# Kernel optimization log

Measured on AMD Instinct MI355X. Metric: run time of the kernel, lower is better.

## Reference

```python
import jax, jax.numpy as jnp
import numpy as np

B, N, R = 4, 16, 64        # batch, permuted axis size, inner spatial size
M, S = N // 2, R * 2       # block count, block size


def _glorot(key, shape):
    fan_in, fan_out = shape[-2], shape[-1]
    lim = np.sqrt(6.0 / (fan_in + fan_out)).astype(np.float32)
    return jax.random.uniform(key, shape, jnp.float32, -lim, lim)


def setup_inputs() -> dict:
    key = jax.random.key(0)
    ks = jax.random.split(key, 10)
    inp = {
        "x": jax.random.normal(ks[0], (B, N, R, N, R, 2), jnp.float32),
        "perm_idx": jax.random.permutation(ks[1], N).astype(jnp.int32),
    }
    for i, name in enumerate(["hr1", "hi1", "hr2", "hi2", "hr3", "hi3", "hr4", "hi4"]):
        inp[name] = _glorot(ks[2 + i], (M, S, S))
    return inp


def _bilin(v, p_right, p_left):
    # v: (B, m, s, m, s). First contract the last s-axis against p_right's
    # block matmuls (block index = axis 3), then the axis-2 s-axis against
    # p_left's block matmuls (block index = axis 1).
    t = jnp.einsum('bmiaj,ajk->bmiak', v, p_right)
    return jnp.einsum('xbjci,bjk->xbkci', t, p_left)


def reference(x, perm_idx, hr1, hi1, hr2, hi2, hr3, hi3, hr4, hi4):
    m = x.shape[1] // 2
    s = x.shape[2] * 2
    n, r = m * 2, s // 2
    x = x.take(perm_idx, axis=1).take(perm_idx, axis=3)
    x = x.reshape((-1, m, s, m, s, 2))
    x_re, x_im = x[..., 0], x[..., 1]

    y_re = (_bilin(x_re, hr1, hr1) + _bilin(x_re, hi1, hi1)
            + _bilin(x_im, hi2, hr2) + _bilin(x_im, hr2, hi2))
    y_im = (_bilin(x_im, hr3, hr3) + _bilin(x_im, hi3, hi3)
            + _bilin(x_re, hi4, hr4) + _bilin(x_re, hr4, hi4))

    y = jnp.stack([y_re, y_im], axis=-1)
    return y.reshape((-1, n, r, n, r, 2))
```

## Files before the change

kernel.cpp:

```cpp
#include <hip/hip_runtime.h>
#include <hip/hip_bf16.h>
#include <stdint.h>

typedef __attribute__((ext_vector_type(8))) short bf16x8;
typedef __attribute__((ext_vector_type(4))) float f32x4;
typedef __attribute__((ext_vector_type(16))) float f32x16;

#define MFMA32(a, b, c) __builtin_amdgcn_mfma_f32_32x32x16_bf16((a), (b), (c), 0, 0, 0)

__device__ __forceinline__ unsigned short f2bf_rn(float f) {
    union { __bf16 b; unsigned short u; } v;
    v.b = (__bf16)f;
    return v.u;
}

__device__ __forceinline__ unsigned int pk2(float lo, float hi) {
    union { unsigned short s[2]; unsigned int u; } r;
    r.s[0] = f2bf_rn(lo); r.s[1] = f2bf_rn(hi);
    return r.u;
}

__device__ __forceinline__ void gload_lds16(const void* g, void* l) {
    __builtin_amdgcn_global_load_lds(
        (const __attribute__((address_space(1))) void*)g,
        (__attribute__((address_space(3))) void*)l, 16, 0, 0);
}

__global__ __launch_bounds__(256) void prep_h(
    const float* __restrict__ h0, const float* __restrict__ h1,
    const float* __restrict__ h2, const float* __restrict__ h3,
    const float* __restrict__ h4, const float* __restrict__ h5,
    const float* __restrict__ h6, const float* __restrict__ h7,
    unsigned short* __restrict__ ht)
{
    const float* hmap[8] = {h0, h1, h2, h3, h4, h5, h6, h7};
    const int wg = blockIdx.x;
    const int jblk = wg >> 2, qt = wg & 3;
    const float* src = hmap[jblk >> 3] + (jblk & 7) * 16384;
    unsigned short* dst = ht + jblk * 16384;
    __shared__ unsigned short tile[32 * 129];
    const int t = threadIdx.x;
    #pragma unroll
    for (int i = 0; i < 16; ++i) {
        int idx = t + 256 * i;
        int r = idx >> 5, kk = idx & 31;
        tile[kk * 129 + r] = f2bf_rn(src[r * 128 + qt * 32 + kk]);
    }
    __syncthreads();
    #pragma unroll
    for (int i = 0; i < 16; ++i) {
        int idx = t + 256 * i;
        int k = idx >> 7, r = idx & 127;
        dst[(qt * 32 + k) * 128 + r] = tile[k * 129 + r];
    }
}

__global__ __launch_bounds__(512, 2) void bilin_main(
    const float* __restrict__ x, const int* __restrict__ perm,
    const unsigned short* __restrict__ ht, float* __restrict__ out)
{
    const int wg = blockIdx.x;
    const int q = wg & 7, p = (wg >> 3) & 7, b = wg >> 6;
    const int tid = threadIdx.x;
    const int lane = tid & 63, wid = tid >> 6;
    const int wn = wid & 3, h = wid >> 2;
    const int l31 = lane & 31, hl = lane >> 5;

    __shared__ __align__(16) unsigned short smem[81920];
    unsigned short* xlds = smem;

    constexpr int cseq[8]  = {0, 1, 6, 7, 2, 3, 4, 5};
    constexpr int rperm[8] = {0, 1, 3, 2, 4, 5, 7, 6};

    const int n1a = perm[2 * p], n1b = perm[2 * p + 1];
    const int n2a = perm[2 * q], n2b = perm[2 * q + 1];

    const int wubase = tid & ~63;
    auto stage_h = [&](unsigned short* dst, int blk) {
        const unsigned short* src = ht + blk * 16384;
        #pragma unroll
        for (int r = 0; r < 4; ++r) {
            const int idx = r * 512 + tid;
            const int row = idx >> 4, cin = idx & 15;
            gload_lds16(src + row * 128 + ((cin ^ (row & 15)) << 3),
                        dst + ((r * 512 + wubase) << 3));
        }
    };

    auto stage_x = [&](int g) {
        float4 xv[4][4];
        int woffs[4];
        #pragma unroll
        for (int i = 0; i < 4; ++i) {
            const int idx = i * 512 + tid;
            const int row = idx >> 4, cin = idx & 15;
            const int n1 = (i >> 1) ? n1b : n1a;
            const int n2 = (cin >> 3) ? n2b : n2a;
            const int r1 = row & 63, r2 = (cin & 7) * 8;
            const float* sp = x + ((size_t)((b * 16 + n1) * 64 + r1) * 1024
                                   + n2 * 64 + r2) * 2;
            #pragma unroll
            for (int j = 0; j < 4; ++j)
                xv[i][j] = *(const float4*)(sp + j * 4);
            woffs[i] = row * 128 + ((cin ^ (row & 15)) << 3);
        }
        #pragma unroll
        for (int i = 0; i < 4; ++i) {
            bf16x8 t;
            #pragma unroll
            for (int j = 0; j < 4; ++j) {
                if (g == 0) {
                    t[2 * j]     = (short)f2bf_rn(xv[i][j].x);
                    t[2 * j + 1] = (short)f2bf_rn(xv[i][j].z);
                } else {
                    t[2 * j]     = (short)f2bf_rn(xv[i][j].y);
                    t[2 * j + 1] = (short)f2bf_rn(xv[i][j].w);
                }
            }
            *(bf16x8*)(xlds + woffs[i]) = t;
        }
    };

    auto ldr = [&](const unsigned short* base, int row, int ch) -> bf16x8 {
        return *(const bf16x8*)(base + row * 128 + ((ch ^ (row & 15)) << 3));
    };

    stage_h(smem + 16384, rperm[0] * 8 + q);
    stage_h(smem + 49152, 0 * 8 + p);
    stage_x(0);
    __syncthreads();

    f32x16 yre[4], yim[4];
    #pragma unroll
    for (int i = 0; i < 4; ++i) {
        #pragma unroll
        for (int e = 0; e < 16; ++e) { yre[i][e] = 0.f; yim[i][e] = 0.f; }
    }

    #pragma unroll
    for (int cc = 0; cc < 8; ++cc) {
        const unsigned short* wb = smem + 16384 + (cc & 1) * 16384;
        const unsigned short* lb = smem + 49152 + (cc & 1) * 16384;

        if (cc < 7) {
            stage_h(smem + 16384 + ((cc + 1) & 1) * 16384,
                    rperm[cseq[cc + 1]] * 8 + q);
            stage_h(smem + 49152 + ((cc + 1) & 1) * 16384,
                    cseq[cc + 1] * 8 + p);
        }

        f32x16 u[2];
        #pragma unroll
        for (int e = 0; e < 16; ++e) { u[0][e] = 0.f; u[1][e] = 0.f; }
        #pragma unroll
        for (int ks = 0; ks < 8; ++ks) {
            bf16x8 wfr = ldr(wb, wn * 32 + l31, 2 * ks + hl);
            #pragma unroll
            for (int m2 = 0; m2 < 2; ++m2) {
                bf16x8 xfr = ldr(xlds, h * 64 + m2 * 32 + l31, 2 * ks + hl);
                u[m2] = MFMA32(xfr, wfr, u[m2]);
            }
        }

        #pragma unroll
        for (int t = 0; t < 4; ++t) {
            const int f = t >> 1, qa = (t & 1) * 2, qb = qa + 1;
            unsigned int lo0 = pk2(u[f][4 * qa + 0], u[f][4 * qa + 1]);
            unsigned int lo1 = pk2(u[f][4 * qa + 2], u[f][4 * qa + 3]);
            unsigned int hi0 = pk2(u[f][4 * qb + 0], u[f][4 * qb + 1]);
            unsigned int hi1 = pk2(u[f][4 * qb + 2], u[f][4 * qb + 3]);
            unsigned int send0 = hl ? lo0 : hi0;
            unsigned int send1 = hl ? lo1 : hi1;
            unsigned int sx0 = (unsigned int)__shfl_xor((int)send0, 32);
            unsigned int sx1 = (unsigned int)__shfl_xor((int)send1, 32);
            union { unsigned int d[4]; bf16x8 v; } ufu;
            ufu.d[0] = hl ? sx0 : lo0;
            ufu.d[1] = hl ? sx1 : lo1;
            ufu.d[2] = hl ? hi0 : sx0;
            ufu.d[3] = hl ? hi1 : sx1;
            #pragma unroll
            for (int mt = 0; mt < 4; ++mt) {
                bf16x8 lfr = ldr(lb, mt * 32 + l31, 8 * h + 2 * t + hl);
                if ((cc & 3) < 2) yre[mt] = MFMA32(lfr, ufu.v, yre[mt]);
                else              yim[mt] = MFMA32(lfr, ufu.v, yim[mt]);
            }
        }

        if (cc == 3) {
            __syncthreads();
            stage_x(1);
        }

        __syncthreads();
    }

    float* red = (float*)smem + wn * 8192;
    if (h == 1) {
        #pragma unroll
        for (int mt = 0; mt < 4; ++mt)
            #pragma unroll
            for (int q4 = 0; q4 < 4; ++q4) {
                f32x4 vr, vi;
                #pragma unroll
                for (int jj = 0; jj < 4; ++jj) {
                    vr[jj] = yre[mt][4 * q4 + jj];
                    vi[jj] = yim[mt][4 * q4 + jj];
                }
                *(f32x4*)(red + ((0 * 4 + mt) * 4 + q4) * 256 + lane * 4) = vr;
                *(f32x4*)(red + ((1 * 4 + mt) * 4 + q4) * 256 + lane * 4) = vi;
            }
    }
    __syncthreads();
    if (h == 0) {
        float2* o2 = (float2*)out;
        #pragma unroll
        for (int mt = 0; mt < 4; ++mt)
            #pragma unroll
            for (int q4 = 0; q4 < 4; ++q4) {
                f32x4 pr = *(const f32x4*)(red + ((0 * 4 + mt) * 4 + q4) * 256 + lane * 4);
                f32x4 pi = *(const f32x4*)(red + ((1 * 4 + mt) * 4 + q4) * 256 + lane * 4);
                #pragma unroll
                for (int jj = 0; jj < 4; ++jj) {
                    const int j = 4 * q4 + jj;
                    const int row = mt * 32 + (j & 3) + 8 * (j >> 2) + 4 * hl;
                    float2 v;
                    v.x = yre[mt][j] + pr[jj];
                    v.y = yim[mt][j] + pi[jj];
                    o2[(size_t)(b * 1024 + p * 128 + row) * 1024
                       + q * 128 + wn * 32 + l31] = v;
                }
            }
    }
}

extern "C" void kernel_launch(void* const* d_in, const int* in_sizes, int n_in,
                              void* d_out, int out_size, void* d_ws, size_t ws_size,
                              hipStream_t stream) {
    const float* x  = (const float*)d_in[0];
    const int* perm = (const int*)d_in[1];
    unsigned short* htp = (unsigned short*)d_ws;

    hipLaunchKernelGGL(prep_h, dim3(256), dim3(256), 0, stream,
        (const float*)d_in[2], (const float*)d_in[3], (const float*)d_in[4],
        (const float*)d_in[5], (const float*)d_in[6], (const float*)d_in[7],
        (const float*)d_in[8], (const float*)d_in[9], htp);
    hipLaunchKernelGGL(bilin_main, dim3(256), dim3(512), 0, stream,
        x, perm, htp, (float*)d_out);
}
```

Before: 40.18 us.

## Use 4-wave workgroups without split-K reduction, register-cached x fragments

Halves the workgroup to 4 waves so each wave computes the full K range for its column strip, which removes the LDS cross-wave reduction at the end. Both real and imaginary x planes are staged once into LDS. The x fragments are held in registers across the loop, reloaded once at the switch to the imaginary plane. The left-matrix buffer is single-buffered and restaged after an extra barrier each iteration. This trades fewer waves per CU and serialized left-matrix loads for less LDS traffic and no reduction pass, and the large register footprint risks spills.

```diff
diff --git a/kernel.cpp b/kernel.cpp
--- a/kernel.cpp
+++ b/kernel.cpp
@@ -55,80 +55,83 @@
     }
 }
 
-__global__ __launch_bounds__(512, 2) void bilin_main(
+__global__ __launch_bounds__(256, 1) void bilin_main(
     const float* __restrict__ x, const int* __restrict__ perm,
     const unsigned short* __restrict__ ht, float* __restrict__ out)
 {
     const int wg = blockIdx.x;
     const int q = wg & 7, p = (wg >> 3) & 7, b = wg >> 6;
     const int tid = threadIdx.x;
-    const int lane = tid & 63, wid = tid >> 6;
-    const int wn = wid & 3, h = wid >> 2;
+    const int lane = tid & 63, wn = tid >> 6;
     const int l31 = lane & 31, hl = lane >> 5;
 
     __shared__ __align__(16) unsigned short smem[81920];
-    unsigned short* xlds = smem;
+    unsigned short* xre_lds = smem;
+    unsigned short* xim_lds = smem + 16384;
+    unsigned short* llds = smem + 65536;
 
     constexpr int cseq[8]  = {0, 1, 6, 7, 2, 3, 4, 5};
     constexpr int rperm[8] = {0, 1, 3, 2, 4, 5, 7, 6};
-
-    const int n1a = perm[2 * p], n1b = perm[2 * p + 1];
-    const int n2a = perm[2 * q], n2b = perm[2 * q + 1];
 
     const int wubase = tid & ~63;
     auto stage_h = [&](unsigned short* dst, int blk) {
         const unsigned short* src = ht + blk * 16384;
         #pragma unroll
-        for (int r = 0; r < 4; ++r) {
-            const int idx = r * 512 + tid;
+        for (int r = 0; r < 8; ++r) {
+            const int idx = r * 256 + tid;
             const int row = idx >> 4, cin = idx & 15;
             gload_lds16(src + row * 128 + ((cin ^ (row & 15)) << 3),
-                        dst + ((r * 512 + wubase) << 3));
-        }
-    };
-
-    auto stage_x = [&](int g) {
-        float4 xv[4][4];
-        int woffs[4];
-        #pragma unroll
-        for (int i = 0; i < 4; ++i) {
-            const int idx = i * 512 + tid;
+                        dst + ((r * 256 + wubase) << 3));
+        }
+    };
+
+    auto ldr = [&](const unsigned short* base, int row, int ch) -> bf16x8 {
+        return *(const bf16x8*)(base + row * 128 + ((ch ^ (row & 15)) << 3));
+    };
+
+    auto stage_x_both = [&]() {
+        #pragma unroll
+        for (int i = 0; i < 8; ++i) {
+            const int idx = i * 256 + tid;
             const int row = idx >> 4, cin = idx & 15;
-            const int n1 = (i >> 1) ? n1b : n1a;
-            const int n2 = (cin >> 3) ? n2b : n2a;
+            const int n1 = perm[2 * p + (row >> 6)];
+            const int n2 = perm[2 * q + (cin >> 3)];
             const int r1 = row & 63, r2 = (cin & 7) * 8;
             const float* sp = x + ((size_t)((b * 16 + n1) * 64 + r1) * 1024
                                    + n2 * 64 + r2) * 2;
-            #pragma unroll
-            for (int j = 0; j < 4; ++j)
-                xv[i][j] = *(const float4*)(sp + j * 4);
-            woffs[i] = row * 128 + ((cin ^ (row & 15)) << 3);
-        }
-        #pragma unroll
-        for (int i = 0; i < 4; ++i) {
-            bf16x8 t;
-            #pragma unroll
-            for (int j = 0; j < 4; ++j) {
-                if (g == 0) {
-                    t[2 * j]     = (short)f2bf_rn(xv[i][j].x);
-                    t[2 * j + 1] = (short)f2bf_rn(xv[i][j].z);
-                } else {
-                    t[2 * j]     = (short)f2bf_rn(xv[i][j].y);
-                    t[2 * j + 1] = (short)f2bf_rn(xv[i][j].w);
-                }
-            }
-            *(bf16x8*)(xlds + woffs[i]) = t;
-        }
-    };
-
-    auto ldr = [&](const unsigned short* base, int row, int ch) -> bf16x8 {
-        return *(const bf16x8*)(base + row * 128 + ((ch ^ (row & 15)) << 3));
-    };
-
-    stage_h(smem + 16384, rperm[0] * 8 + q);
-    stage_h(smem + 49152, 0 * 8 + p);
-    stage_x(0);
+            float4 v0 = *(const float4*)(sp);
+            float4 v1 = *(const float4*)(sp + 4);
+            float4 v2 = *(const float4*)(sp + 8);
+            float4 v3 = *(const float4*)(sp + 12);
+            bf16x8 re, im;
+            re[0] = (short)f2bf_rn(v0.x); re[1] = (short)f2bf_rn(v0.z);
+            re[2] = (short)f2bf_rn(v1.x); re[3] = (short)f2bf_rn(v1.z);
+            re[4] = (short)f2bf_rn(v2.x); re[5] = (short)f2bf_rn(v2.z);
+            re[6] = (short)f2bf_rn(v3.x); re[7] = (short)f2bf_rn(v3.z);
+            im[0] = (short)f2bf_rn(v0.y); im[1] = (short)f2bf_rn(v0.w);
+            im[2] = (short)f2bf_rn(v1.y); im[3] = (short)f2bf_rn(v1.w);
+            im[4] = (short)f2bf_rn(v2.y); im[5] = (short)f2bf_rn(v2.w);
+            im[6] = (short)f2bf_rn(v3.y); im[7] = (short)f2bf_rn(v3.w);
+            const int woff = row * 128 + ((cin ^ (row & 15)) << 3);
+            *(bf16x8*)(xre_lds + woff) = re;
+            *(bf16x8*)(xim_lds + woff) = im;
+        }
+    };
+
+    bf16x8 xf[4][8];
+    auto load_xf = [&](const unsigned short* plane) {
+        #pragma unroll
+        for (int m2 = 0; m2 < 4; ++m2)
+            #pragma unroll
+            for (int ks = 0; ks < 8; ++ks)
+                xf[m2][ks] = ldr(plane, m2 * 32 + l31, 2 * ks + hl);
+    };
+
+    stage_h(smem + 32768, rperm[0] * 8 + q);
+    stage_h(llds, 0 * 8 + p);
+    stage_x_both();
     __syncthreads();
+    load_xf(xre_lds);
 
     f32x16 yre[4], yim[4];
     #pragma unroll
@@ -139,31 +142,31 @@
 
     #pragma unroll
     for (int cc = 0; cc < 8; ++cc) {
-        const unsigned short* wb = smem + 16384 + (cc & 1) * 16384;
-        const unsigned short* lb = smem + 49152 + (cc & 1) * 16384;
-
-        if (cc < 7) {
-            stage_h(smem + 16384 + ((cc + 1) & 1) * 16384,
+        const unsigned short* wb = smem + 32768 + (cc & 1) * 16384;
+
+        if (cc < 7)
+            stage_h(smem + 32768 + ((cc + 1) & 1) * 16384,
                     rperm[cseq[cc + 1]] * 8 + q);
-            stage_h(smem + 49152 + ((cc + 1) & 1) * 16384,
-                    cseq[cc + 1] * 8 + p);
-        }
-
-        f32x16 u[2];
-        #pragma unroll
-        for (int e = 0; e < 16; ++e) { u[0][e] = 0.f; u[1][e] = 0.f; }
+
+        if (cc == 4) load_xf(xim_lds);
+
+        f32x16 u[4];
+        #pragma unroll
+        for (int m2 = 0; m2 < 4; ++m2)
+            #pragma unroll
+            for (int e = 0; e < 16; ++e) u[m2][e] = 0.f;
         #pragma unroll
         for (int ks = 0; ks < 8; ++ks) {
             bf16x8 wfr = ldr(wb, wn * 32 + l31, 2 * ks + hl);
             #pragma unroll
-            for (int m2 = 0; m2 < 2; ++m2) {
-                bf16x8 xfr = ldr(xlds, h * 64 + m2 * 32 + l31, 2 * ks + hl);
-                u[m2] = MFMA32(xfr, wfr, u[m2]);
-            }
-        }
-
-        #pragma unroll
-        for (int t = 0; t < 4; ++t) {
+            for (int m2 = 0; m2 < 4; ++m2)
+                u[m2] = MFMA32(xf[m2][ks], wfr, u[m2]);
+        }
+
+        __syncthreads();
+
+        #pragma unroll
+        for (int t = 0; t < 8; ++t) {
             const int f = t >> 1, qa = (t & 1) * 2, qb = qa + 1;
             unsigned int lo0 = pk2(u[f][4 * qa + 0], u[f][4 * qa + 1]);
             unsigned int lo1 = pk2(u[f][4 * qa + 2], u[f][4 * qa + 3]);
@@ -180,57 +183,29 @@
             ufu.d[3] = hl ? hi1 : sx1;
             #pragma unroll
             for (int mt = 0; mt < 4; ++mt) {
-                bf16x8 lfr = ldr(lb, mt * 32 + l31, 8 * h + 2 * t + hl);
+                bf16x8 lfr = ldr(llds, mt * 32 + l31, 2 * t + hl);
                 if ((cc & 3) < 2) yre[mt] = MFMA32(lfr, ufu.v, yre[mt]);
                 else              yim[mt] = MFMA32(lfr, ufu.v, yim[mt]);
             }
         }
 
-        if (cc == 3) {
-            __syncthreads();
-            stage_x(1);
-        }
-
         __syncthreads();
-    }
-
-    float* red = (float*)smem + wn * 8192;
-    if (h == 1) {
-        #pragma unroll
-        for (int mt = 0; mt < 4; ++mt)
-            #pragma unroll
-            for (int q4 = 0; q4 < 4; ++q4) {
-                f32x4 vr, vi;
-                #pragma unroll
-                for (int jj = 0; jj < 4; ++jj) {
-                    vr[jj] = yre[mt][4 * q4 + jj];
-                    vi[jj] = yim[mt][4 * q4 + jj];
-                }
-                *(f32x4*)(red + ((0 * 4 + mt) * 4 + q4) * 256 + lane * 4) = vr;
-                *(f32x4*)(red + ((1 * 4 + mt) * 4 + q4) * 256 + lane * 4) = vi;
-            }
-    }
-    __syncthreads();
-    if (h == 0) {
-        float2* o2 = (float2*)out;
-        #pragma unroll
-        for (int mt = 0; mt < 4; ++mt)
-            #pragma unroll
-            for (int q4 = 0; q4 < 4; ++q4) {
-                f32x4 pr = *(const f32x4*)(red + ((0 * 4 + mt) * 4 + q4) * 256 + lane * 4);
-                f32x4 pi = *(const f32x4*)(red + ((1 * 4 + mt) * 4 + q4) * 256 + lane * 4);
-                #pragma unroll
-                for (int jj = 0; jj < 4; ++jj) {
-                    const int j = 4 * q4 + jj;
-                    const int row = mt * 32 + (j & 3) + 8 * (j >> 2) + 4 * hl;
-                    float2 v;
-                    v.x = yre[mt][j] + pr[jj];
-                    v.y = yim[mt][j] + pi[jj];
-                    o2[(size_t)(b * 1024 + p * 128 + row) * 1024
-                       + q * 128 + wn * 32 + l31] = v;
-                }
-            }
-    }
+        if (cc < 7)
+            stage_h(llds, cseq[cc + 1] * 8 + p);
+    }
+
+    float2* o2 = (float2*)out;
+    #pragma unroll
+    for (int mt = 0; mt < 4; ++mt)
+        #pragma unroll
+        for (int j = 0; j < 16; ++j) {
+            const int row = mt * 32 + (j & 3) + 8 * (j >> 2) + 4 * hl;
+            float2 v;
+            v.x = yre[mt][j];
+            v.y = yim[mt][j];
+            o2[(size_t)(b * 1024 + p * 128 + row) * 1024
+               + q * 128 + wn * 32 + l31] = v;
+        }
 }
 
 extern "C" void kernel_launch(void* const* d_in, const int* in_sizes, int n_in,
@@ -244,6 +219,6 @@
         (const float*)d_in[2], (const float*)d_in[3], (const float*)d_in[4],
         (const float*)d_in[5], (const float*)d_in[6], (const float*)d_in[7],
         (const float*)d_in[8], (const float*)d_in[9], htp);
-    hipLaunchKernelGGL(bilin_main, dim3(256), dim3(512), 0, stream,
+    hipLaunchKernelGGL(bilin_main, dim3(256), dim3(256), 0, stream,
         x, perm, htp, (float*)d_out);
 }
```

After: 39.48 us. Within noise of the previous version (-1.7%).
